# Kernel tuning notes

Hardware: AMD Instinct MI355X
Metric: run time of the kernel (lower is better)

Reference implementation:

```python
import jax, jax.numpy as jnp
import numpy as np

B, S, D, H = 2, 1024, 1024, 8
HD = D // H            # head_dim = 128
NBUCKETS = 64          # bucket_size (number of hash buckets)
NEG = -1e30


def setup_inputs() -> dict:
    key = jax.random.key(0)
    ks = jax.random.split(key, 10)
    scale = D ** -0.5
    return {
        "x": jax.random.normal(ks[0], (B, S, D), dtype=jnp.float32),
        "Wq": jax.random.normal(ks[1], (D, D), dtype=jnp.float32) * scale,
        "bq": jnp.zeros((D,), dtype=jnp.float32),
        "Wk": jax.random.normal(ks[2], (D, D), dtype=jnp.float32) * scale,
        "bk": jnp.zeros((D,), dtype=jnp.float32),
        "Wv": jax.random.normal(ks[3], (D, D), dtype=jnp.float32) * scale,
        "bv": jnp.zeros((D,), dtype=jnp.float32),
        "Wo": jax.random.normal(ks[4], (D, D), dtype=jnp.float32) * scale,
        "bo": jnp.zeros((D,), dtype=jnp.float32),
        "hash_proj": jax.random.normal(ks[5], (H, HD, NBUCKETS), dtype=jnp.float32),
    }


def reference(x, Wq, bq, Wk, bk, Wv, bv, Wo, bo, hash_proj):
    b, s, d = x.shape
    n = b * s  # buckets gather (batch, token) pairs jointly -> flatten batch into tokens

    def split_heads(y):  # [B,S,D] -> [H, B*S, HD]
        return y.reshape(b, s, H, HD).transpose(2, 0, 1, 3).reshape(H, n, HD)

    q = split_heads(x @ Wq + bq)
    k = split_heads(x @ Wk + bk)
    v = split_heads(x @ Wv + bv)

    # learned LSH routing: argmax over hash projections per head
    hash_scores = jnp.einsum('hnd,hdf->hnf', q, hash_proj)
    buckets = jnp.argmax(hash_scores, axis=-1)  # [H, N] int

    # per-bucket attention == masked dense attention with same-bucket mask
    dots = jnp.einsum('hnd,hmd->hnm', q, k) / (HD ** 0.5)  # [H,N,N]
    same = buckets[:, :, None] == buckets[:, None, :]
    attn = jax.nn.softmax(jnp.where(same, dots, NEG), axis=-1)
    o = jnp.einsum('hnm,hmd->hnd', attn, v)  # [H,N,HD]

    out = o.reshape(H, b, s, HD).transpose(1, 2, 0, 3).reshape(b, s, d)
    return out @ Wo + bo
```

## Files before the change

kernel.cpp:

```cpp
#include <hip/hip_runtime.h>
#include <stdint.h>

typedef __attribute__((ext_vector_type(8))) short short8;
typedef __attribute__((ext_vector_type(4))) short short4v;
typedef __attribute__((ext_vector_type(4))) float float4v;
typedef unsigned short u16;

#define N_TOK 2048
#define D_MODEL 1024
#define N_HEAD 8
#define HDIM 128
#define N_BUCKET 64
#define WL_CAP 2048
#define ATTN_BLOCKS 384

__device__ __forceinline__ u16 f2bf(float f) {
  uint32_t u = __float_as_uint(f);
  uint32_t r = u + 0x7fffu + ((u >> 16) & 1u);
  return (u16)(r >> 16);
}
__device__ __forceinline__ float bf2f(u16 h) {
  return __uint_as_float(((uint32_t)h) << 16);
}

__device__ __forceinline__ void async_load16(const void* g, void* l) {
  __builtin_amdgcn_global_load_lds(
      (const __attribute__((address_space(1))) void*)g,
      (__attribute__((address_space(3))) void*)l, 16, 0, 0);
}

__device__ __forceinline__ int xcd_swz(int bid, int nwg) {
  return (bid & 7) * (nwg >> 3) + (bid >> 3);
}

__global__ __launch_bounds__(256) void split_cast_kernel(
    const float* __restrict__ in, u16* __restrict__ hi, u16* __restrict__ lo,
    int n) {
  int i = blockIdx.x * 256 + threadIdx.x;
  if (i >= n) return;
  float v = in[i];
  u16 h = f2bf(v);
  hi[i] = h;
  if (lo) lo[i] = f2bf(v - bf2f(h));
}

__global__ __launch_bounds__(256) void transpose_all_kernel(
    const float* __restrict__ Wq, const float* __restrict__ Wk,
    const float* __restrict__ Wv, const float* __restrict__ Wo,
    u16* __restrict__ wqt_hi, u16* __restrict__ wqt_lo,
    u16* __restrict__ kvt, u16* __restrict__ wot) {
  __shared__ float tile[32][33];
  const int z = blockIdx.z;
  const float* in = (z == 0) ? Wq : (z == 1) ? Wk : (z == 2) ? Wv : Wo;
  u16* hi = (z == 0) ? wqt_hi
            : (z == 1) ? kvt
            : (z == 2) ? (kvt + (size_t)1024 * 1024) : wot;
  u16* lo = (z == 0) ? wqt_lo : nullptr;
  const int C = 1024, R = 1024;
  int c0 = blockIdx.x * 32, r0 = blockIdx.y * 32;
  int tx = threadIdx.x & 31, ty = threadIdx.x >> 5;
#pragma unroll
  for (int i = 0; i < 4; i++) {
    int rl = ty + i * 8;
    tile[rl][tx] = in[(size_t)(r0 + rl) * C + c0 + tx];
  }
  __syncthreads();
#pragma unroll
  for (int i = 0; i < 4; i++) {
    int cl = ty + i * 8;
    float v = tile[tx][cl];
    size_t oidx = (size_t)(c0 + cl) * R + r0 + tx;
    u16 h = f2bf(v);
    hi[oidx] = h;
    if (lo) lo[oidx] = f2bf(v - bf2f(h));
  }
}

template <int BM>
__device__ __forceinline__ void stage_tiles2(const u16* A, const u16* Bt,
                                             u16* As, u16* Bs, int bm, int bn,
                                             int K, int ko, int wave, int lane) {
  const int arow = lane >> 2;
  const int acolb = (lane & 3) * 16;
  constexpr int ACH = BM / 16;
  constexpr int PC = (ACH + 8) / 4;
#pragma unroll
  for (int cc = 0; cc < PC; cc++) {
    int idx = wave * PC + cc;
    if (idx < ACH) {
      int row = idx * 16 + arow;
      const char* g = (const char*)A + ((size_t)(bm + row) * K + ko) * 2 + acolb;
      async_load16(g, (char*)As + idx * 1024);
    } else {
      int row = (idx - ACH) * 16 + arow;
      const char* g = (const char*)Bt + ((size_t)(bn + row) * K + ko) * 2 + acolb;
      async_load16(g, (char*)Bs + (idx - ACH) * 1024);
    }
  }
}

template <int BM>
__global__ __launch_bounds__(256) void gemm_bf16_kernel(
    const u16* __restrict__ A, const u16* __restrict__ Bt,
    float* __restrict__ C, const float* __restrict__ bias,
    const float* __restrict__ bias2, u16* __restrict__ kbf,
    u16* __restrict__ vbf, int N, int K, int flags) {
  constexpr int MI = BM / 32;
  __shared__ __align__(16) u16 As[2][BM * 32];
  __shared__ __align__(16) u16 Bs[2][128 * 32];
  const int tid = threadIdx.x;
  const int wave = tid >> 6, lane = tid & 63;
  const int lhi = lane >> 4, llo = lane & 15;
  const int nbn = N >> 7;
  const int bid = xcd_swz(blockIdx.x, gridDim.x);
  const int bm = (bid / nbn) * BM;
  const int bn = (bid % nbn) << 7;
  const int wm = (BM == 128) ? (wave >> 1) * 64 : (wave & 1) * 32;
  const int wn = (BM == 128) ? (wave & 1) * 64 : (wave >> 1) * 64;

  float4v acc[MI][4];
#pragma unroll
  for (int mi = 0; mi < MI; mi++)
#pragma unroll
    for (int ni = 0; ni < 4; ni++)
#pragma unroll
      for (int r = 0; r < 4; r++) acc[mi][ni][r] = 0.f;

  stage_tiles2<BM>(A, Bt, As[0], Bs[0], bm, bn, K, 0, wave, lane);
  __syncthreads();
  const int nk = K >> 5;
  for (int t = 0; t < nk; t++) {
    const int cur = t & 1;
    if (t + 1 < nk)
      stage_tiles2<BM>(A, Bt, As[cur ^ 1], Bs[cur ^ 1], bm, bn, K,
                       (t + 1) << 5, wave, lane);
    short8 af[MI], bfr[4];
#pragma unroll
    for (int i = 0; i < MI; i++)
      af[i] = *(const short8*)&As[cur][(wm + i * 16 + llo) * 32 + lhi * 8];
#pragma unroll
    for (int i = 0; i < 4; i++)
      bfr[i] = *(const short8*)&Bs[cur][(wn + i * 16 + llo) * 32 + lhi * 8];
#pragma unroll
    for (int mi = 0; mi < MI; mi++)
#pragma unroll
      for (int ni = 0; ni < 4; ni++)
        acc[mi][ni] = __builtin_amdgcn_mfma_f32_16x16x32_bf16(af[mi], bfr[ni],
                                                              acc[mi][ni], 0, 0, 0);
    __syncthreads();
  }

#pragma unroll
  for (int mi = 0; mi < MI; mi++)
#pragma unroll
    for (int ni = 0; ni < 4; ni++) {
      int row0 = bm + wm + mi * 16 + lhi * 4;
      int col = bn + wn + ni * 16 + llo;
      if (flags & 8) {
        u16* dst = (col < 1024) ? kbf : vbf;
        int c = col & 1023;
        float bb = (col < 1024) ? bias[c] : bias2[c];
#pragma unroll
        for (int r = 0; r < 4; r++)
          dst[(size_t)(row0 + r) * 1024 + c] = f2bf(acc[mi][ni][r] + bb);
      } else {
        float bb = (flags & 2) ? bias[col] : 0.f;
        float* cp = C + (size_t)row0 * N + col;
#pragma unroll
        for (int r = 0; r < 4; r++) cp[(size_t)r * N] = acc[mi][ni][r] + bb;
      }
    }
}

__global__ __launch_bounds__(256) void gemm3_bf16_kernel(
    const u16* __restrict__ A0, const u16* __restrict__ A1,
    const u16* __restrict__ B0, const u16* __restrict__ B1,
    float* __restrict__ C, const float* __restrict__ bias,
    u16* __restrict__ bf_out, int N, int K) {
  constexpr int MI = 2;
  __shared__ __align__(16) u16 S3[2][12288];
  const int tid = threadIdx.x;
  const int wave = tid >> 6, lane = tid & 63;
  const int lhi = lane >> 4, llo = lane & 15;
  const int nbn = N >> 7;
  const int bid = xcd_swz(blockIdx.x, gridDim.x);
  const int bm = (bid / nbn) * 64;
  const int bn = (bid % nbn) << 7;
  const int wm = (wave & 1) * 32;
  const int wn = (wave >> 1) * 64;
  const int arow = lane >> 2;
  const int acolb = (lane & 3) * 16;

  float4v acc[MI][4];
#pragma unroll
  for (int mi = 0; mi < MI; mi++)
#pragma unroll
    for (int ni = 0; ni < 4; ni++)
#pragma unroll
      for (int r = 0; r < 4; r++) acc[mi][ni][r] = 0.f;

  auto stage = [&](int b, int ko) {
    char* base = (char*)&S3[b][0];
#pragma unroll
    for (int cc = 0; cc < 6; cc++) {
      int idx = wave * 6 + cc;
      const u16* src;
      int row;
      char* dst;
      if (idx < 4) {
        src = A0; row = bm + idx * 16 + arow; dst = base + idx * 1024;
      } else if (idx < 8) {
        src = A1; row = bm + (idx - 4) * 16 + arow; dst = base + 4096 + (idx - 4) * 1024;
      } else if (idx < 16) {
        src = B0; row = bn + (idx - 8) * 16 + arow; dst = base + 8192 + (idx - 8) * 1024;
      } else {
        src = B1; row = bn + (idx - 16) * 16 + arow; dst = base + 16384 + (idx - 16) * 1024;
      }
      async_load16((const char*)src + ((size_t)row * K + ko) * 2 + acolb, dst);
    }
  };

  stage(0, 0);
  __syncthreads();
  const int nk = K >> 5;
  for (int t = 0; t < nk; t++) {
    const int cur = t & 1;
    if (t + 1 < nk) stage(cur ^ 1, (t + 1) << 5);
    const u16* Sc = &S3[cur][0];
    short8 afh[MI], afl[MI], bfh[4], bfl[4];
#pragma unroll
    for (int i = 0; i < MI; i++) {
      afh[i] = *(const short8*)&Sc[(wm + i * 16 + llo) * 32 + lhi * 8];
      afl[i] = *(const short8*)&Sc[2048 + (wm + i * 16 + llo) * 32 + lhi * 8];
    }
#pragma unroll
    for (int i = 0; i < 4; i++) {
      bfh[i] = *(const short8*)&Sc[4096 + (wn + i * 16 + llo) * 32 + lhi * 8];
      bfl[i] = *(const short8*)&Sc[8192 + (wn + i * 16 + llo) * 32 + lhi * 8];
    }
#pragma unroll
    for (int mi = 0; mi < MI; mi++)
#pragma unroll
      for (int ni = 0; ni < 4; ni++)
        acc[mi][ni] = __builtin_amdgcn_mfma_f32_16x16x32_bf16(afh[mi], bfh[ni],
                                                              acc[mi][ni], 0, 0, 0);
#pragma unroll
    for (int mi = 0; mi < MI; mi++)
#pragma unroll
      for (int ni = 0; ni < 4; ni++)
        acc[mi][ni] = __builtin_amdgcn_mfma_f32_16x16x32_bf16(afh[mi], bfl[ni],
                                                              acc[mi][ni], 0, 0, 0);
#pragma unroll
    for (int mi = 0; mi < MI; mi++)
#pragma unroll
      for (int ni = 0; ni < 4; ni++)
        acc[mi][ni] = __builtin_amdgcn_mfma_f32_16x16x32_bf16(afl[mi], bfh[ni],
                                                              acc[mi][ni], 0, 0, 0);
    __syncthreads();
  }

#pragma unroll
  for (int mi = 0; mi < MI; mi++)
#pragma unroll
    for (int ni = 0; ni < 4; ni++) {
      int row0 = bm + wm + mi * 16 + lhi * 4;
      int col = bn + wn + ni * 16 + llo;
      float bb = bias[col];
#pragma unroll
      for (int r = 0; r < 4; r++) {
        float v = acc[mi][ni][r] + bb;
        C[(size_t)(row0 + r) * N + col] = v;
        bf_out[(size_t)(row0 + r) * N + col] = f2bf(v);
      }
    }
}

__global__ __launch_bounds__(256) void hash_argmax_kernel(
    const float* __restrict__ Qf, const float* __restrict__ proj,
    int* __restrict__ bucket) {
  __shared__ float sQ[64 * 128];
  __shared__ float sP[128 * 64];
  const int tid = threadIdx.x;
  const int h = blockIdx.y;
  const int n0 = blockIdx.x * 64;
#pragma unroll
  for (int p = 0; p < 8; p++) {
    int e = p * 1024 + tid * 4;
    int tok = e >> 7, d0 = e & 127;
    float4v v = *(const float4v*)&Qf[(size_t)(n0 + tok) * D_MODEL + h * HDIM + d0];
    int blk = (d0 >> 2) ^ ((tok >> 2) & 7);
    *(float4v*)&sQ[tok * 128 + blk * 4] = v;
  }
#pragma unroll
  for (int p = 0; p < 8; p++) {
    int e = p * 1024 + tid * 4;
    float4v v = *(const float4v*)&proj[(size_t)h * (HDIM * N_BUCKET) + e];
    *(float4v*)&sP[e] = v;
  }
  __syncthreads();

  const int tgrp = tid & 15, fgrp = tid >> 4;
  const int t0 = tgrp * 4, f0 = fgrp * 4;
  float accs[4][4];
#pragma unroll
  for (int i = 0; i < 4; i++)
#pragma unroll
    for (int f = 0; f < 4; f++) accs[i][f] = 0.f;

  for (int d0 = 0; d0 < 128; d0 += 4) {
    int blk = (d0 >> 2) ^ (tgrp & 7);
    float4v qv[4], pv[4];
#pragma unroll
    for (int i = 0; i < 4; i++)
      qv[i] = *(const float4v*)&sQ[(t0 + i) * 128 + blk * 4];
#pragma unroll
    for (int j = 0; j < 4; j++)
      pv[j] = *(const float4v*)&sP[(d0 + j) * 64 + f0];
#pragma unroll
    for (int i = 0; i < 4; i++)
#pragma unroll
      for (int f = 0; f < 4; f++)
        accs[i][f] += qv[i][0] * pv[0][f] + qv[i][1] * pv[1][f] +
                      qv[i][2] * pv[2][f] + qv[i][3] * pv[3][f];
  }

  __syncthreads();
  float* vals = sQ;
  int* idxs = (int*)(sQ + 64 * 17);
#pragma unroll
  for (int i = 0; i < 4; i++) {
    float bv = accs[i][0];
    int bi = f0;
#pragma unroll
    for (int f = 1; f < 4; f++)
      if (accs[i][f] > bv) { bv = accs[i][f]; bi = f0 + f; }
    vals[(t0 + i) * 17 + fgrp] = bv;
    idxs[(t0 + i) * 17 + fgrp] = bi;
  }
  __syncthreads();
  if (tid < 64) {
    float bv = vals[tid * 17];
    int bi = idxs[tid * 17];
#pragma unroll
    for (int g = 1; g < 16; g++) {
      float v = vals[tid * 17 + g];
      int id = idxs[tid * 17 + g];
      if (v > bv || (v == bv && id < bi)) { bv = v; bi = id; }
    }
    bucket[h * N_TOK + n0 + tid] = bi;
  }
}

__global__ __launch_bounds__(64) void bucket_count_kernel(
    const int* __restrict__ bucket, int* __restrict__ counts) {
  int hb = blockIdx.x;
  int h = hb >> 6, b = hb & 63;
  int lane = threadIdx.x;
  int cnt = 0;
  for (int t = 0; t < N_TOK; t += 64) {
    bool match = bucket[h * N_TOK + t + lane] == b;
    unsigned long long mask = __ballot(match);
    cnt += __popcll(mask);
  }
  if (lane == 0) counts[hb] = cnt;
}

__global__ __launch_bounds__(512) void build_wl_kernel(
    const int* __restrict__ counts, int* __restrict__ offsets,
    int* __restrict__ wl, int* __restrict__ wl_count) {
  __shared__ int sc[512];
  int tid = threadIdx.x;
  int cnt = counts[tid];
  sc[tid] = cnt;
  __syncthreads();
  for (int o = 1; o < 512; o <<= 1) {
    int v = (tid >= o) ? sc[tid - o] : 0;
    __syncthreads();
    sc[tid] += v;
    __syncthreads();
  }
  offsets[tid] = sc[tid] - cnt;
  __syncthreads();
  int nq = (cnt + 15) >> 4;
  sc[tid] = nq;
  __syncthreads();
  for (int o = 1; o < 512; o <<= 1) {
    int v = (tid >= o) ? sc[tid - o] : 0;
    __syncthreads();
    sc[tid] += v;
    __syncthreads();
  }
  int base = sc[tid] - nq;
  int h = tid >> 6, b = tid & 63;
  for (int i = 0; i < nq; i++) wl[base + i] = (h << 13) | (b << 7) | i;
  if (tid == 511) wl_count[0] = sc[511];
}

__global__ __launch_bounds__(64) void bucket_fill_kernel(
    const int* __restrict__ bucket, const int* __restrict__ offsets,
    int* __restrict__ perm) {
  int hb = blockIdx.x;
  int h = hb >> 6, b = hb & 63;
  int lane = threadIdx.x;
  int base = offsets[hb];
  for (int t = 0; t < N_TOK; t += 64) {
    int tok = t + lane;
    bool match = bucket[h * N_TOK + tok] == b;
    unsigned long long mask = __ballot(match);
    if (match) {
      int pos = base + __popcll(mask & ((1ull << lane) - 1ull));
      perm[pos] = tok;
    }
    base += __popcll(mask);
  }
}

__global__ __launch_bounds__(256) void gather_vt_kernel(
    const u16* __restrict__ vbb, const int* __restrict__ perm,
    u16* __restrict__ Vts) {
  __shared__ u16 lds[64][72];
  int bid = blockIdx.x;
  int h = bid >> 6;
  int ptile = (bid & 63) >> 1;
  int d0 = (bid & 1) * 64;
  int pos0 = ptile * 64;
  int t = threadIdx.x;
#pragma unroll
  for (int i = 0; i < 2; i++) {
    int unit = t + 256 * i;
    int p = unit >> 3, seg = unit & 7;
    int tok = perm[h * N_TOK + pos0 + p];
    short8 v = *(const short8*)&vbb[(size_t)tok * D_MODEL + h * HDIM + d0 + seg * 8];
    *(short8*)&lds[p][seg * 8] = v;
  }
  __syncthreads();
#pragma unroll
  for (int i = 0; i < 8; i++) {
    int unit = t + 256 * i;
    int drow = unit >> 5, pp = unit & 31;
    uint32_t val = (uint32_t)lds[2 * pp][drow] |
                   ((uint32_t)lds[2 * pp + 1][drow] << 16);
    uint32_t* dst = (uint32_t*)&Vts[(size_t)(h * HDIM + d0 + drow) * N_TOK + pos0];
    dst[pp] = val;
  }
}

__global__ __launch_bounds__(256) void attn_bucket_kernel(
    const u16* __restrict__ qbb, const u16* __restrict__ kbb,
    const u16* __restrict__ Vts, const int* __restrict__ perm,
    const int* __restrict__ offsets, const int* __restrict__ counts,
    const int* __restrict__ wl, const int* __restrict__ wl_count,
    u16* __restrict__ ob) {
  const int wave = threadIdx.x >> 6, lane = threadIdx.x & 63;
  const int lhi = lane >> 4, llo = lane & 15;
  const int wslot = blockIdx.x * 4 + wave;
  const int NW = ATTN_BLOCKS * 4;
  const int cnt = wl_count[0];
  __shared__ __align__(16) u16 P_lds[4][16][64];
  const float scale = 0.08838834764831845f;

  for (int e = wslot; e < cnt; e += NW) {
    int ent = wl[e];
    int h = ent >> 13, qt = ent & 127;
    int hb = (h << 6) | ((ent >> 7) & 63);
    int off = offsets[hb];
    int bs = counts[hb];
    int offh = off - h * N_TOK;
    int qbase = qt * 16;

    int qr = qbase + llo;
    int tokq = perm[off + min(qr, bs - 1)];
    const u16* qrow = &qbb[(size_t)tokq * D_MODEL + h * HDIM];
    short8 qf[4];
#pragma unroll
    for (int kf = 0; kf < 4; kf++)
      qf[kf] = *(const short8*)&qrow[kf * 32 + lhi * 8];

    float m[4], l[4];
#pragma unroll
    for (int r = 0; r < 4; r++) { m[r] = -INFINITY; l[r] = 0.f; }
    float4v accO[8];
#pragma unroll
    for (int d = 0; d < 8; d++)
#pragma unroll
      for (int r = 0; r < 4; r++) accO[d][r] = 0.f;

    for (int c0 = 0; c0 < bs; c0 += 64) {
      float4v sc[4];
#pragma unroll
      for (int nf = 0; nf < 4; nf++)
#pragma unroll
        for (int r = 0; r < 4; r++) sc[nf][r] = 0.f;
#pragma unroll
      for (int nf = 0; nf < 4; nf++) {
        int kcol = c0 + nf * 16 + llo;
        int tokk = perm[off + min(kcol, bs - 1)];
        const u16* krow = &kbb[(size_t)tokk * D_MODEL + h * HDIM];
#pragma unroll
        for (int kf = 0; kf < 4; kf++) {
          short8 kfr = *(const short8*)&krow[kf * 32 + lhi * 8];
          sc[nf] = __builtin_amdgcn_mfma_f32_16x16x32_bf16(qf[kf], kfr, sc[nf], 0, 0, 0);
        }
      }

      float tmax[4];
#pragma unroll
      for (int r = 0; r < 4; r++) tmax[r] = -INFINITY;
#pragma unroll
      for (int nf = 0; nf < 4; nf++) {
        bool valid = (c0 + nf * 16 + llo) < bs;
#pragma unroll
        for (int r = 0; r < 4; r++) {
          float v = valid ? sc[nf][r] * scale : -1e30f;
          sc[nf][r] = v;
          tmax[r] = fmaxf(tmax[r], v);
        }
      }
#pragma unroll
      for (int r = 0; r < 4; r++)
#pragma unroll
        for (int o = 1; o < 16; o <<= 1)
          tmax[r] = fmaxf(tmax[r], __shfl_xor(tmax[r], o));

      float resc[4], psum[4];
#pragma unroll
      for (int r = 0; r < 4; r++) {
        float mn = fmaxf(m[r], tmax[r]);
        resc[r] = __expf(m[r] - mn);
        m[r] = mn;
        psum[r] = 0.f;
      }
#pragma unroll
      for (int nf = 0; nf < 4; nf++)
#pragma unroll
        for (int r = 0; r < 4; r++) {
          float p = __expf(sc[nf][r] - m[r]);
          psum[r] += p;
          P_lds[wave][lhi * 4 + r][nf * 16 + llo] = f2bf(p);
        }
#pragma unroll
      for (int r = 0; r < 4; r++) {
#pragma unroll
        for (int o = 1; o < 16; o <<= 1) psum[r] += __shfl_xor(psum[r], o);
        l[r] = l[r] * resc[r] + psum[r];
      }
#pragma unroll
      for (int d = 0; d < 8; d++)
#pragma unroll
        for (int r = 0; r < 4; r++) accO[d][r] *= resc[r];

      asm volatile("s_waitcnt lgkmcnt(0)" ::: "memory");
      short8 pf[2];
#pragma unroll
      for (int k2 = 0; k2 < 2; k2++)
        pf[k2] = *(const short8*)&P_lds[wave][llo][k2 * 32 + lhi * 8];
#pragma unroll
      for (int d = 0; d < 8; d++)
#pragma unroll
        for (int k2 = 0; k2 < 2; k2++) {
          short8 vfr = *(const short8*)&Vts[(size_t)(h * HDIM + d * 16 + llo) * N_TOK +
                                            offh + c0 + k2 * 32 + lhi * 8];
          accO[d] = __builtin_amdgcn_mfma_f32_16x16x32_bf16(pf[k2], vfr, accO[d], 0, 0, 0);
        }
      asm volatile("" ::: "memory");
    }

#pragma unroll
    for (int r = 0; r < 4; r++) {
      int rl = qbase + lhi * 4 + r;
      if (rl < bs) {
        int tok = perm[off + rl];
        float inv = 1.f / l[r];
#pragma unroll
        for (int d = 0; d < 8; d++)
          ob[(size_t)tok * D_MODEL + h * HDIM + d * 16 + llo] = f2bf(accO[d][r] * inv);
      }
    }
  }
}

extern "C" void kernel_launch(void* const* d_in, const int* in_sizes, int n_in,
                              void* d_out, int out_size, void* d_ws, size_t ws_size,
                              hipStream_t stream) {
  const float* x  = (const float*)d_in[0];
  const float* Wq = (const float*)d_in[1];
  const float* bq = (const float*)d_in[2];
  const float* Wk = (const float*)d_in[3];
  const float* bk = (const float*)d_in[4];
  const float* Wv = (const float*)d_in[5];
  const float* bv = (const float*)d_in[6];
  const float* Wo = (const float*)d_in[7];
  const float* bo = (const float*)d_in[8];
  const float* hp = (const float*)d_in[9];
  float* out = (float*)d_out;

  char* ws = (char*)d_ws;
  size_t off = 0;
  auto alloc = [&](size_t b) {
    char* p = ws + off;
    off += (b + 255) & ~(size_t)255;
    return p;
  };

  const int N = N_TOK, D = D_MODEL;
  u16* xhi    = (u16*)alloc((size_t)N * D * 2);
  u16* xlo    = (u16*)alloc((size_t)N * D * 2);
  u16* wqt_hi = (u16*)alloc((size_t)D * D * 2);
  u16* wqt_lo = (u16*)alloc((size_t)D * D * 2);
  u16* kvt    = (u16*)alloc((size_t)2 * D * D * 2);
  u16* wot    = (u16*)alloc((size_t)D * D * 2);
  float* Qf   = (float*)alloc((size_t)N * D * 4);
  u16* qbb    = (u16*)alloc((size_t)N * D * 2);
  u16* kbb    = (u16*)alloc((size_t)N * D * 2);
  u16* vbb    = (u16*)alloc((size_t)N * D * 2);
  u16* Vts    = (u16*)alloc((size_t)N_HEAD * HDIM * N * 2 + 256);
  int* bucket = (int*)alloc((size_t)N_HEAD * N * 4);
  int* counts = (int*)alloc(512 * 4);
  int* offs   = (int*)alloc(512 * 4);
  int* perm   = (int*)alloc((size_t)N_HEAD * N * 4);
  int* wl     = (int*)alloc(WL_CAP * 4);
  int* wlcnt  = (int*)alloc(256);
  u16* ob     = (u16*)alloc((size_t)N * D * 2);

  const int nelem = N * D;

  split_cast_kernel<<<(nelem + 255) / 256, 256, 0, stream>>>(x, xhi, xlo, nelem);
  transpose_all_kernel<<<dim3(32, 32, 4), 256, 0, stream>>>(
      Wq, Wk, Wv, Wo, wqt_hi, wqt_lo, kvt, wot);

  gemm3_bf16_kernel<<<(N / 64) * (D / 128), 256, 0, stream>>>(
      xhi, xlo, wqt_hi, wqt_lo, Qf, bq, qbb, D, D);
  gemm_bf16_kernel<64><<<(N / 64) * (2 * D / 128), 256, 0, stream>>>(
      xhi, kvt, nullptr, bk, bv, kbb, vbb, 2 * D, D, 2 | 8);

  hash_argmax_kernel<<<dim3(N / 64, N_HEAD), 256, 0, stream>>>(Qf, hp, bucket);
  bucket_count_kernel<<<512, 64, 0, stream>>>(bucket, counts);
  build_wl_kernel<<<1, 512, 0, stream>>>(counts, offs, wl, wlcnt);
  bucket_fill_kernel<<<512, 64, 0, stream>>>(bucket, offs, perm);
  gather_vt_kernel<<<512, 256, 0, stream>>>(vbb, perm, Vts);

  attn_bucket_kernel<<<ATTN_BLOCKS, 256, 0, stream>>>(
      qbb, kbb, Vts, perm, offs, counts, wl, wlcnt, ob);

  gemm_bf16_kernel<64><<<(N / 64) * (D / 128), 256, 0, stream>>>(
      ob, wot, out, bo, nullptr, nullptr, nullptr, D, D, 2);

  (void)in_sizes; (void)n_in; (void)out_size; (void)ws_size;
}
```

Measured before the change: 131.7 us.

## Fold hash projection into Wq and merge QKV GEMM and bucket sort kernels

New measurement: 161.4 us. 1.23x slower.

```diff
diff --git a/kernel.cpp b/kernel.cpp
--- a/kernel.cpp
+++ b/kernel.cpp
@@ -47,15 +47,11 @@
 __global__ __launch_bounds__(256) void transpose_all_kernel(
     const float* __restrict__ Wq, const float* __restrict__ Wk,
     const float* __restrict__ Wv, const float* __restrict__ Wo,
-    u16* __restrict__ wqt_hi, u16* __restrict__ wqt_lo,
-    u16* __restrict__ kvt, u16* __restrict__ wot) {
+    u16* __restrict__ qkvt, u16* __restrict__ wot) {
   __shared__ float tile[32][33];
   const int z = blockIdx.z;
   const float* in = (z == 0) ? Wq : (z == 1) ? Wk : (z == 2) ? Wv : Wo;
-  u16* hi = (z == 0) ? wqt_hi
-            : (z == 1) ? kvt
-            : (z == 2) ? (kvt + (size_t)1024 * 1024) : wot;
-  u16* lo = (z == 0) ? wqt_lo : nullptr;
+  u16* hi = (z == 3) ? wot : qkvt + (size_t)z * 1024 * 1024;
   const int C = 1024, R = 1024;
   int c0 = blockIdx.x * 32, r0 = blockIdx.y * 32;
   int tx = threadIdx.x & 31, ty = threadIdx.x >> 5;
@@ -68,81 +64,120 @@
 #pragma unroll
   for (int i = 0; i < 4; i++) {
     int cl = ty + i * 8;
-    float v = tile[tx][cl];
-    size_t oidx = (size_t)(c0 + cl) * R + r0 + tx;
-    u16 h = f2bf(v);
-    hi[oidx] = h;
-    if (lo) lo[oidx] = f2bf(v - bf2f(h));
-  }
-}
-
-template <int BM>
-__device__ __forceinline__ void stage_tiles2(const u16* A, const u16* Bt,
-                                             u16* As, u16* Bs, int bm, int bn,
-                                             int K, int ko, int wave, int lane) {
-  const int arow = lane >> 2;
-  const int acolb = (lane & 3) * 16;
-  constexpr int ACH = BM / 16;
-  constexpr int PC = (ACH + 8) / 4;
-#pragma unroll
-  for (int cc = 0; cc < PC; cc++) {
-    int idx = wave * PC + cc;
-    if (idx < ACH) {
-      int row = idx * 16 + arow;
-      const char* g = (const char*)A + ((size_t)(bm + row) * K + ko) * 2 + acolb;
-      async_load16(g, (char*)As + idx * 1024);
-    } else {
-      int row = (idx - ACH) * 16 + arow;
-      const char* g = (const char*)Bt + ((size_t)(bn + row) * K + ko) * 2 + acolb;
-      async_load16(g, (char*)Bs + (idx - ACH) * 1024);
-    }
-  }
-}
-
-template <int BM>
-__global__ __launch_bounds__(256) void gemm_bf16_kernel(
+    hi[(size_t)(c0 + cl) * R + r0 + tx] = f2bf(tile[tx][cl]);
+  }
+}
+
+__global__ __launch_bounds__(256) void wqp_build_kernel(
+    const float* __restrict__ Wq, const float* __restrict__ proj,
+    const float* __restrict__ bq, u16* __restrict__ Wqpt_hi,
+    u16* __restrict__ Wqpt_lo, float* __restrict__ bias_sc) {
+  __shared__ float sW[64][128];
+  __shared__ float sPj[128][64];
+  const int tid = threadIdx.x;
+  const int rt = blockIdx.x, h = blockIdx.y;
+  const int dd0 = rt * 64;
+#pragma unroll
+  for (int p = 0; p < 8; p++) {
+    int e = p * 1024 + tid * 4;
+    int row = e >> 7, col = e & 127;
+    *(float4v*)&sW[row][col] =
+        *(const float4v*)&Wq[(size_t)(dd0 + row) * 1024 + h * HDIM + col];
+    *(float4v*)&sPj[0][0 + e] = *(const float4v*)&proj[(size_t)h * (HDIM * N_BUCKET) + e];
+  }
+  __syncthreads();
+  const int tr0 = (tid & 15) * 4, tc0 = (tid >> 4) * 4;
+  float acc[4][4];
+#pragma unroll
+  for (int i = 0; i < 4; i++)
+#pragma unroll
+    for (int j = 0; j < 4; j++) acc[i][j] = 0.f;
+  for (int dl = 0; dl < 128; dl++) {
+    float4v pv = *(const float4v*)&sPj[dl][tc0];
+#pragma unroll
+    for (int i = 0; i < 4; i++) {
+      float w = sW[tr0 + i][dl];
+#pragma unroll
+      for (int j = 0; j < 4; j++) acc[i][j] += w * pv[j];
+    }
+  }
+#pragma unroll
+  for (int j = 0; j < 4; j++) {
+    short4v ph, pl;
+#pragma unroll
+    for (int i = 0; i < 4; i++) {
+      float v = acc[i][j];
+      u16 hh = f2bf(v);
+      ph[i] = (short)hh;
+      pl[i] = (short)f2bf(v - bf2f(hh));
+    }
+    size_t ofs = (size_t)(h * 64 + tc0 + j) * 1024 + dd0 + tr0;
+    *(short4v*)&Wqpt_hi[ofs] = ph;
+    *(short4v*)&Wqpt_lo[ofs] = pl;
+  }
+  if (rt == 0 && tid < 64) {
+    float s = 0.f;
+    for (int dl = 0; dl < 128; dl++) s += bq[h * HDIM + dl] * sPj[dl][tid];
+    bias_sc[h * 64 + tid] = s;
+  }
+}
+
+__global__ __launch_bounds__(256) void qkv_gemm_kernel(
     const u16* __restrict__ A, const u16* __restrict__ Bt,
-    float* __restrict__ C, const float* __restrict__ bias,
-    const float* __restrict__ bias2, u16* __restrict__ kbf,
-    u16* __restrict__ vbf, int N, int K, int flags) {
-  constexpr int MI = BM / 32;
-  __shared__ __align__(16) u16 As[2][BM * 32];
+    const float* __restrict__ bq, const float* __restrict__ bk,
+    const float* __restrict__ bv, u16* __restrict__ qbb,
+    u16* __restrict__ kbb, u16* __restrict__ vbb) {
+  const int K = 1024;
+  __shared__ __align__(16) u16 As[2][128 * 32];
   __shared__ __align__(16) u16 Bs[2][128 * 32];
   const int tid = threadIdx.x;
   const int wave = tid >> 6, lane = tid & 63;
   const int lhi = lane >> 4, llo = lane & 15;
-  const int nbn = N >> 7;
   const int bid = xcd_swz(blockIdx.x, gridDim.x);
-  const int bm = (bid / nbn) * BM;
-  const int bn = (bid % nbn) << 7;
-  const int wm = (BM == 128) ? (wave >> 1) * 64 : (wave & 1) * 32;
-  const int wn = (BM == 128) ? (wave & 1) * 64 : (wave >> 1) * 64;
-
-  float4v acc[MI][4];
-#pragma unroll
-  for (int mi = 0; mi < MI; mi++)
+  const int bm = (bid / 24) << 7;
+  const int bn = (bid % 24) << 7;
+  const int wm = (wave >> 1) * 64;
+  const int wn = (wave & 1) * 64;
+  const int arow = lane >> 2;
+  const int acolb = (lane & 3) * 16;
+
+  float4v acc[4][4];
+#pragma unroll
+  for (int mi = 0; mi < 4; mi++)
 #pragma unroll
     for (int ni = 0; ni < 4; ni++)
 #pragma unroll
       for (int r = 0; r < 4; r++) acc[mi][ni][r] = 0.f;
 
-  stage_tiles2<BM>(A, Bt, As[0], Bs[0], bm, bn, K, 0, wave, lane);
-  __syncthreads();
-  const int nk = K >> 5;
-  for (int t = 0; t < nk; t++) {
+  auto stage = [&](int b, int ko) {
+#pragma unroll
+    for (int cc = 0; cc < 4; cc++) {
+      int idx = wave * 4 + cc;
+      if (idx < 8) {
+        int row = bm + idx * 16 + arow;
+        async_load16((const char*)A + ((size_t)row * K + ko) * 2 + acolb,
+                     (char*)&As[b][0] + idx * 1024);
+      } else {
+        int row = bn + (idx - 8) * 16 + arow;
+        async_load16((const char*)Bt + ((size_t)row * K + ko) * 2 + acolb,
+                     (char*)&Bs[b][0] + (idx - 8) * 1024);
+      }
+    }
+  };
+
+  stage(0, 0);
+  __syncthreads();
+  for (int t = 0; t < 32; t++) {
     const int cur = t & 1;
-    if (t + 1 < nk)
-      stage_tiles2<BM>(A, Bt, As[cur ^ 1], Bs[cur ^ 1], bm, bn, K,
-                       (t + 1) << 5, wave, lane);
-    short8 af[MI], bfr[4];
-#pragma unroll
-    for (int i = 0; i < MI; i++)
+    if (t + 1 < 32) stage(cur ^ 1, (t + 1) << 5);
+    short8 af[4], bfr[4];
+#pragma unroll
+    for (int i = 0; i < 4; i++) {
       af[i] = *(const short8*)&As[cur][(wm + i * 16 + llo) * 32 + lhi * 8];
-#pragma unroll
-    for (int i = 0; i < 4; i++)
       bfr[i] = *(const short8*)&Bs[cur][(wn + i * 16 + llo) * 32 + lhi * 8];
-#pragma unroll
-    for (int mi = 0; mi < MI; mi++)
+    }
+#pragma unroll
+    for (int mi = 0; mi < 4; mi++)
 #pragma unroll
       for (int ni = 0; ni < 4; ni++)
         acc[mi][ni] = __builtin_amdgcn_mfma_f32_16x16x32_bf16(af[mi], bfr[ni],
@@ -151,70 +186,59 @@
   }
 
 #pragma unroll
-  for (int mi = 0; mi < MI; mi++)
+  for (int mi = 0; mi < 4; mi++)
 #pragma unroll
     for (int ni = 0; ni < 4; ni++) {
       int row0 = bm + wm + mi * 16 + lhi * 4;
       int col = bn + wn + ni * 16 + llo;
-      if (flags & 8) {
-        u16* dst = (col < 1024) ? kbf : vbf;
-        int c = col & 1023;
-        float bb = (col < 1024) ? bias[c] : bias2[c];
-#pragma unroll
-        for (int r = 0; r < 4; r++)
-          dst[(size_t)(row0 + r) * 1024 + c] = f2bf(acc[mi][ni][r] + bb);
-      } else {
-        float bb = (flags & 2) ? bias[col] : 0.f;
-        float* cp = C + (size_t)row0 * N + col;
-#pragma unroll
-        for (int r = 0; r < 4; r++) cp[(size_t)r * N] = acc[mi][ni][r] + bb;
-      }
-    }
-}
-
-__global__ __launch_bounds__(256) void gemm3_bf16_kernel(
+      int seg = col >> 10, c = col & 1023;
+      u16* dst = (seg == 0) ? qbb : (seg == 1) ? kbb : vbb;
+      float bb = (seg == 0) ? bq[c] : (seg == 1) ? bk[c] : bv[c];
+#pragma unroll
+      for (int r = 0; r < 4; r++)
+        dst[(size_t)(row0 + r) * 1024 + c] = f2bf(acc[mi][ni][r] + bb);
+    }
+}
+
+__global__ __launch_bounds__(256) void score_argmax_kernel(
     const u16* __restrict__ A0, const u16* __restrict__ A1,
     const u16* __restrict__ B0, const u16* __restrict__ B1,
-    float* __restrict__ C, const float* __restrict__ bias,
-    u16* __restrict__ bf_out, int N, int K) {
-  constexpr int MI = 2;
-  __shared__ __align__(16) u16 S3[2][12288];
+    const float* __restrict__ bias_sc, int* __restrict__ bucket) {
+  const int K = 1024;
+  __shared__ __align__(16) u16 S[2][10240];
   const int tid = threadIdx.x;
   const int wave = tid >> 6, lane = tid & 63;
   const int lhi = lane >> 4, llo = lane & 15;
-  const int nbn = N >> 7;
   const int bid = xcd_swz(blockIdx.x, gridDim.x);
-  const int bm = (bid / nbn) * 64;
-  const int bn = (bid % nbn) << 7;
-  const int wm = (wave & 1) * 32;
+  const int bm = (bid >> 2) << 5;
+  const int bn = (bid & 3) << 7;
+  const int wm = (wave & 1) * 16;
   const int wn = (wave >> 1) * 64;
   const int arow = lane >> 2;
   const int acolb = (lane & 3) * 16;
 
-  float4v acc[MI][4];
-#pragma unroll
-  for (int mi = 0; mi < MI; mi++)
-#pragma unroll
-    for (int ni = 0; ni < 4; ni++)
-#pragma unroll
-      for (int r = 0; r < 4; r++) acc[mi][ni][r] = 0.f;
+  float4v acc[4];
+#pragma unroll
+  for (int ni = 0; ni < 4; ni++)
+#pragma unroll
+    for (int r = 0; r < 4; r++) acc[ni][r] = 0.f;
 
   auto stage = [&](int b, int ko) {
-    char* base = (char*)&S3[b][0];
-#pragma unroll
-    for (int cc = 0; cc < 6; cc++) {
-      int idx = wave * 6 + cc;
+    char* base = (char*)&S[b][0];
+#pragma unroll
+    for (int cc = 0; cc < 5; cc++) {
+      int idx = wave * 5 + cc;
       const u16* src;
       int row;
       char* dst;
-      if (idx < 4) {
+      if (idx < 2) {
         src = A0; row = bm + idx * 16 + arow; dst = base + idx * 1024;
-      } else if (idx < 8) {
-        src = A1; row = bm + (idx - 4) * 16 + arow; dst = base + 4096 + (idx - 4) * 1024;
-      } else if (idx < 16) {
-        src = B0; row = bn + (idx - 8) * 16 + arow; dst = base + 8192 + (idx - 8) * 1024;
+      } else if (idx < 4) {
+        src = A1; row = bm + (idx - 2) * 16 + arow; dst = base + 2048 + (idx - 2) * 1024;
+      } else if (idx < 12) {
+        src = B0; row = bn + (idx - 4) * 16 + arow; dst = base + 4096 + (idx - 4) * 1024;
       } else {
-        src = B1; row = bn + (idx - 16) * 16 + arow; dst = base + 16384 + (idx - 16) * 1024;
+        src = B1; row = bn + (idx - 12) * 16 + arow; dst = base + 12288 + (idx - 12) * 1024;
       }
       async_load16((const char*)src + ((size_t)row * K + ko) * 2 + acolb, dst);
     }
@@ -222,156 +246,82 @@
 
   stage(0, 0);
   __syncthreads();
-  const int nk = K >> 5;
-  for (int t = 0; t < nk; t++) {
+  for (int t = 0; t < 32; t++) {
     const int cur = t & 1;
-    if (t + 1 < nk) stage(cur ^ 1, (t + 1) << 5);
-    const u16* Sc = &S3[cur][0];
-    short8 afh[MI], afl[MI], bfh[4], bfl[4];
-#pragma unroll
-    for (int i = 0; i < MI; i++) {
-      afh[i] = *(const short8*)&Sc[(wm + i * 16 + llo) * 32 + lhi * 8];
-      afl[i] = *(const short8*)&Sc[2048 + (wm + i * 16 + llo) * 32 + lhi * 8];
-    }
+    if (t + 1 < 32) stage(cur ^ 1, (t + 1) << 5);
+    const u16* Sc = &S[cur][0];
+    short8 afh, afl, bfh[4], bfl[4];
+    afh = *(const short8*)&Sc[(wm + llo) * 32 + lhi * 8];
+    afl = *(const short8*)&Sc[1024 + (wm + llo) * 32 + lhi * 8];
 #pragma unroll
     for (int i = 0; i < 4; i++) {
-      bfh[i] = *(const short8*)&Sc[4096 + (wn + i * 16 + llo) * 32 + lhi * 8];
-      bfl[i] = *(const short8*)&Sc[8192 + (wn + i * 16 + llo) * 32 + lhi * 8];
-    }
-#pragma unroll
-    for (int mi = 0; mi < MI; mi++)
-#pragma unroll
-      for (int ni = 0; ni < 4; ni++)
-        acc[mi][ni] = __builtin_amdgcn_mfma_f32_16x16x32_bf16(afh[mi], bfh[ni],
-                                                              acc[mi][ni], 0, 0, 0);
-#pragma unroll
-    for (int mi = 0; mi < MI; mi++)
-#pragma unroll
-      for (int ni = 0; ni < 4; ni++)
-        acc[mi][ni] = __builtin_amdgcn_mfma_f32_16x16x32_bf16(afh[mi], bfl[ni],
-                                                              acc[mi][ni], 0, 0, 0);
-#pragma unroll
-    for (int mi = 0; mi < MI; mi++)
-#pragma unroll
-      for (int ni = 0; ni < 4; ni++)
-        acc[mi][ni] = __builtin_amdgcn_mfma_f32_16x16x32_bf16(afl[mi], bfh[ni],
-                                                              acc[mi][ni], 0, 0, 0);
+      bfh[i] = *(const short8*)&Sc[2048 + (wn + i * 16 + llo) * 32 + lhi * 8];
+      bfl[i] = *(const short8*)&Sc[6144 + (wn + i * 16 + llo) * 32 + lhi * 8];
+    }
+#pragma unroll
+    for (int ni = 0; ni < 4; ni++)
+      acc[ni] = __builtin_amdgcn_mfma_f32_16x16x32_bf16(afh, bfh[ni], acc[ni], 0, 0, 0);
+#pragma unroll
+    for (int ni = 0; ni < 4; ni++)
+      acc[ni] = __builtin_amdgcn_mfma_f32_16x16x32_bf16(afh, bfl[ni], acc[ni], 0, 0, 0);
+#pragma unroll
+    for (int ni = 0; ni < 4; ni++)
+      acc[ni] = __builtin_amdgcn_mfma_f32_16x16x32_bf16(afl, bfh[ni], acc[ni], 0, 0, 0);
     __syncthreads();
   }
 
-#pragma unroll
-  for (int mi = 0; mi < MI; mi++)
-#pragma unroll
-    for (int ni = 0; ni < 4; ni++) {
-      int row0 = bm + wm + mi * 16 + lhi * 4;
-      int col = bn + wn + ni * 16 + llo;
-      float bb = bias[col];
-#pragma unroll
-      for (int r = 0; r < 4; r++) {
-        float v = acc[mi][ni][r] + bb;
-        C[(size_t)(row0 + r) * N + col] = v;
-        bf_out[(size_t)(row0 + r) * N + col] = f2bf(v);
-      }
-    }
-}
-
-__global__ __launch_bounds__(256) void hash_argmax_kernel(
-    const float* __restrict__ Qf, const float* __restrict__ proj,
-    int* __restrict__ bucket) {
-  __shared__ float sQ[64 * 128];
-  __shared__ float sP[128 * 64];
+  const int head = (bn + wn) >> 6;
+  float bsc[4];
+#pragma unroll
+  for (int ni = 0; ni < 4; ni++) bsc[ni] = bias_sc[head * 64 + ni * 16 + llo];
+#pragma unroll
+  for (int r = 0; r < 4; r++) {
+    float bv = acc[0][r] + bsc[0];
+    int bi = llo;
+#pragma unroll
+    for (int ni = 1; ni < 4; ni++) {
+      float v = acc[ni][r] + bsc[ni];
+      if (v > bv) { bv = v; bi = ni * 16 + llo; }
+    }
+#pragma unroll
+    for (int o = 1; o < 16; o <<= 1) {
+      float ov = __shfl_xor(bv, o);
+      int oi = __shfl_xor(bi, o);
+      if (ov > bv || (ov == bv && oi < bi)) { bv = ov; bi = oi; }
+    }
+    if (llo == 0) bucket[head * N_TOK + bm + wm + lhi * 4 + r] = bi;
+  }
+}
+
+__device__ __forceinline__ unsigned long long match_mask(int b) {
+  unsigned long long mask = ~0ull;
+#pragma unroll
+  for (int bit = 0; bit < 6; bit++) {
+    unsigned long long vt = __ballot((b >> bit) & 1);
+    mask &= ((b >> bit) & 1) ? vt : ~vt;
+  }
+  return mask;
+}
+
+__global__ __launch_bounds__(512) void sort_kernel(
+    const int* __restrict__ bucket, int* __restrict__ counts_g,
+    int* __restrict__ offsets_g, int* __restrict__ perm,
+    int* __restrict__ wl, int* __restrict__ wl_count) {
+  __shared__ int cnt[512];
+  __shared__ int sc[512];
+  __shared__ int run[512];
   const int tid = threadIdx.x;
-  const int h = blockIdx.y;
-  const int n0 = blockIdx.x * 64;
-#pragma unroll
-  for (int p = 0; p < 8; p++) {
-    int e = p * 1024 + tid * 4;
-    int tok = e >> 7, d0 = e & 127;
-    float4v v = *(const float4v*)&Qf[(size_t)(n0 + tok) * D_MODEL + h * HDIM + d0];
-    int blk = (d0 >> 2) ^ ((tok >> 2) & 7);
-    *(float4v*)&sQ[tok * 128 + blk * 4] = v;
-  }
-#pragma unroll
-  for (int p = 0; p < 8; p++) {
-    int e = p * 1024 + tid * 4;
-    float4v v = *(const float4v*)&proj[(size_t)h * (HDIM * N_BUCKET) + e];
-    *(float4v*)&sP[e] = v;
-  }
-  __syncthreads();
-
-  const int tgrp = tid & 15, fgrp = tid >> 4;
-  const int t0 = tgrp * 4, f0 = fgrp * 4;
-  float accs[4][4];
-#pragma unroll
-  for (int i = 0; i < 4; i++)
-#pragma unroll
-    for (int f = 0; f < 4; f++) accs[i][f] = 0.f;
-
-  for (int d0 = 0; d0 < 128; d0 += 4) {
-    int blk = (d0 >> 2) ^ (tgrp & 7);
-    float4v qv[4], pv[4];
-#pragma unroll
-    for (int i = 0; i < 4; i++)
-      qv[i] = *(const float4v*)&sQ[(t0 + i) * 128 + blk * 4];
-#pragma unroll
-    for (int j = 0; j < 4; j++)
-      pv[j] = *(const float4v*)&sP[(d0 + j) * 64 + f0];
-#pragma unroll
-    for (int i = 0; i < 4; i++)
-#pragma unroll
-      for (int f = 0; f < 4; f++)
-        accs[i][f] += qv[i][0] * pv[0][f] + qv[i][1] * pv[1][f] +
-                      qv[i][2] * pv[2][f] + qv[i][3] * pv[3][f];
-  }
-
-  __syncthreads();
-  float* vals = sQ;
-  int* idxs = (int*)(sQ + 64 * 17);
-#pragma unroll
-  for (int i = 0; i < 4; i++) {
-    float bv = accs[i][0];
-    int bi = f0;
-#pragma unroll
-    for (int f = 1; f < 4; f++)
-      if (accs[i][f] > bv) { bv = accs[i][f]; bi = f0 + f; }
-    vals[(t0 + i) * 17 + fgrp] = bv;
-    idxs[(t0 + i) * 17 + fgrp] = bi;
-  }
-  __syncthreads();
-  if (tid < 64) {
-    float bv = vals[tid * 17];
-    int bi = idxs[tid * 17];
-#pragma unroll
-    for (int g = 1; g < 16; g++) {
-      float v = vals[tid * 17 + g];
-      int id = idxs[tid * 17 + g];
-      if (v > bv || (v == bv && id < bi)) { bv = v; bi = id; }
-    }
-    bucket[h * N_TOK + n0 + tid] = bi;
-  }
-}
-
-__global__ __launch_bounds__(64) void bucket_count_kernel(
-    const int* __restrict__ bucket, int* __restrict__ counts) {
-  int hb = blockIdx.x;
-  int h = hb >> 6, b = hb & 63;
-  int lane = threadIdx.x;
-  int cnt = 0;
+  const int w = tid >> 6, lane = tid & 63;
+  cnt[tid] = 0;
+  __syncthreads();
   for (int t = 0; t < N_TOK; t += 64) {
-    bool match = bucket[h * N_TOK + t + lane] == b;
-    unsigned long long mask = __ballot(match);
-    cnt += __popcll(mask);
-  }
-  if (lane == 0) counts[hb] = cnt;
-}
-
-__global__ __launch_bounds__(512) void build_wl_kernel(
-    const int* __restrict__ counts, int* __restrict__ offsets,
-    int* __restrict__ wl, int* __restrict__ wl_count) {
-  __shared__ int sc[512];
-  int tid = threadIdx.x;
-  int cnt = counts[tid];
-  sc[tid] = cnt;
+    int b = bucket[w * N_TOK + t + lane];
+    unsigned long long mask = match_mask(b);
+    if (lane == __ffsll(mask) - 1) cnt[w * 64 + b] += __popcll(mask);
+  }
+  __syncthreads();
+  int c = cnt[tid];
+  sc[tid] = c;
   __syncthreads();
   for (int o = 1; o < 512; o <<= 1) {
     int v = (tid >= o) ? sc[tid - o] : 0;
@@ -379,9 +329,12 @@
     sc[tid] += v;
     __syncthreads();
   }
-  offsets[tid] = sc[tid] - cnt;
-  __syncthreads();
-  int nq = (cnt + 15) >> 4;
+  int off0 = sc[tid] - c;
+  offsets_g[tid] = off0;
+  counts_g[tid] = c;
+  run[tid] = off0;
+  __syncthreads();
+  int nq = (c + 15) >> 4;
   sc[tid] = nq;
   __syncthreads();
   for (int o = 1; o < 512; o <<= 1) {
@@ -391,27 +344,18 @@
     __syncthreads();
   }
   int base = sc[tid] - nq;
-  int h = tid >> 6, b = tid & 63;
-  for (int i = 0; i < nq; i++) wl[base + i] = (h << 13) | (b << 7) | i;
+  int hh = tid >> 6, bb = tid & 63;
+  for (int i = 0; i < nq; i++) wl[base + i] = (hh << 13) | (bb << 7) | i;
   if (tid == 511) wl_count[0] = sc[511];
-}
-
-__global__ __launch_bounds__(64) void bucket_fill_kernel(
-    const int* __restrict__ bucket, const int* __restrict__ offsets,
-    int* __restrict__ perm) {
-  int hb = blockIdx.x;
-  int h = hb >> 6, b = hb & 63;
-  int lane = threadIdx.x;
-  int base = offsets[hb];
+  __syncthreads();
   for (int t = 0; t < N_TOK; t += 64) {
     int tok = t + lane;
-    bool match = bucket[h * N_TOK + tok] == b;
-    unsigned long long mask = __ballot(match);
-    if (match) {
-      int pos = base + __popcll(mask & ((1ull << lane) - 1ull));
-      perm[pos] = tok;
-    }
-    base += __popcll(mask);
+    int b = bucket[w * N_TOK + tok];
+    unsigned long long mask = match_mask(b);
+    int lower = __popcll(mask & ((1ull << lane) - 1ull));
+    int pos = run[w * 64 + b] + lower;
+    perm[pos] = tok;
+    if (lane == __ffsll(mask) - 1) run[w * 64 + b] += __popcll(mask);
   }
 }
 
@@ -486,11 +430,11 @@
       for (int r = 0; r < 4; r++) accO[d][r] = 0.f;
 
     for (int c0 = 0; c0 < bs; c0 += 64) {
-      float4v sc[4];
+      float4v scv[4];
 #pragma unroll
       for (int nf = 0; nf < 4; nf++)
 #pragma unroll
-        for (int r = 0; r < 4; r++) sc[nf][r] = 0.f;
+        for (int r = 0; r < 4; r++) scv[nf][r] = 0.f;
 #pragma unroll
       for (int nf = 0; nf < 4; nf++) {
         int kcol = c0 + nf * 16 + llo;
@@ -499,7 +443,7 @@
 #pragma unroll
         for (int kf = 0; kf < 4; kf++) {
           short8 kfr = *(const short8*)&krow[kf * 32 + lhi * 8];
-          sc[nf] = __builtin_amdgcn_mfma_f32_16x16x32_bf16(qf[kf], kfr, sc[nf], 0, 0, 0);
+          scv[nf] = __builtin_amdgcn_mfma_f32_16x16x32_bf16(qf[kf], kfr, scv[nf], 0, 0, 0);
         }
       }
 
@@ -511,8 +455,8 @@
         bool valid = (c0 + nf * 16 + llo) < bs;
 #pragma unroll
         for (int r = 0; r < 4; r++) {
-          float v = valid ? sc[nf][r] * scale : -1e30f;
-          sc[nf][r] = v;
+          float v = valid ? scv[nf][r] * scale : -1e30f;
+          scv[nf][r] = v;
           tmax[r] = fmaxf(tmax[r], v);
         }
       }
@@ -534,7 +478,7 @@
       for (int nf = 0; nf < 4; nf++)
 #pragma unroll
         for (int r = 0; r < 4; r++) {
-          float p = __expf(sc[nf][r] - m[r]);
+          float p = __expf(scv[nf][r] - m[r]);
           psum[r] += p;
           P_lds[wave][lhi * 4 + r][nf * 16 + llo] = f2bf(p);
         }
@@ -577,6 +521,81 @@
       }
     }
   }
+}
+
+__global__ __launch_bounds__(256) void gemm_out_kernel(
+    const u16* __restrict__ A, const u16* __restrict__ Bt,
+    float* __restrict__ C, const float* __restrict__ bias) {
+  const int K = 1024, N = 1024;
+  __shared__ __align__(16) u16 As[2][64 * 32];
+  __shared__ __align__(16) u16 Bs[2][128 * 32];
+  const int tid = threadIdx.x;
+  const int wave = tid >> 6, lane = tid & 63;
+  const int lhi = lane >> 4, llo = lane & 15;
+  const int bid = xcd_swz(blockIdx.x, gridDim.x);
+  const int bm = (bid >> 3) * 64;
+  const int bn = (bid & 7) << 7;
+  const int wm = (wave & 1) * 32;
+  const int wn = (wave >> 1) * 64;
+  const int arow = lane >> 2;
+  const int acolb = (lane & 3) * 16;
+
+  float4v acc[2][4];
+#pragma unroll
+  for (int mi = 0; mi < 2; mi++)
+#pragma unroll
+    for (int ni = 0; ni < 4; ni++)
+#pragma unroll
+      for (int r = 0; r < 4; r++) acc[mi][ni][r] = 0.f;
+
+  auto stage = [&](int b, int ko) {
+#pragma unroll
+    for (int cc = 0; cc < 3; cc++) {
+      int idx = wave * 3 + cc;
+      if (idx < 4) {
+        int row = bm + idx * 16 + arow;
+        async_load16((const char*)A + ((size_t)row * K + ko) * 2 + acolb,
+                     (char*)&As[b][0] + idx * 1024);
+      } else {
+        int row = bn + (idx - 4) * 16 + arow;
+        async_load16((const char*)Bt + ((size_t)row * K + ko) * 2 + acolb,
+                     (char*)&Bs[b][0] + (idx - 4) * 1024);
+      }
+    }
+  };
+
+  stage(0, 0);
+  __syncthreads();
+  for (int t = 0; t < 32; t++) {
+    const int cur = t & 1;
+    if (t + 1 < 32) stage(cur ^ 1, (t + 1) << 5);
+    short8 af[2], bfr[4];
+#pragma unroll
+    for (int i = 0; i < 2; i++)
+      af[i] = *(const short8*)&As[cur][(wm + i * 16 + llo) * 32 + lhi * 8];
+#pragma unroll
+    for (int i = 0; i < 4; i++)
+      bfr[i] = *(const short8*)&Bs[cur][(wn + i * 16 + llo) * 32 + lhi * 8];
+#pragma unroll
+    for (int mi = 0; mi < 2; mi++)
+#pragma unroll
+      for (int ni = 0; ni < 4; ni++)
+        acc[mi][ni] = __builtin_amdgcn_mfma_f32_16x16x32_bf16(af[mi], bfr[ni],
+                                                              acc[mi][ni], 0, 0, 0);
+    __syncthreads();
+  }
+
+#pragma unroll
+  for (int mi = 0; mi < 2; mi++)
+#pragma unroll
+    for (int ni = 0; ni < 4; ni++) {
+      int row0 = bm + wm + mi * 16 + lhi * 4;
+      int col = bn + wn + ni * 16 + llo;
+      float bb = bias[col];
+#pragma unroll
+      for (int r = 0; r < 4; r++)
+        C[(size_t)(row0 + r) * N + col] = acc[mi][ni][r] + bb;
+    }
 }
 
 extern "C" void kernel_launch(void* const* d_in, const int* in_sizes, int n_in,
@@ -603,47 +622,41 @@
   };
 
   const int N = N_TOK, D = D_MODEL;
-  u16* xhi    = (u16*)alloc((size_t)N * D * 2);
-  u16* xlo    = (u16*)alloc((size_t)N * D * 2);
-  u16* wqt_hi = (u16*)alloc((size_t)D * D * 2);
-  u16* wqt_lo = (u16*)alloc((size_t)D * D * 2);
-  u16* kvt    = (u16*)alloc((size_t)2 * D * D * 2);
-  u16* wot    = (u16*)alloc((size_t)D * D * 2);
-  float* Qf   = (float*)alloc((size_t)N * D * 4);
-  u16* qbb    = (u16*)alloc((size_t)N * D * 2);
-  u16* kbb    = (u16*)alloc((size_t)N * D * 2);
-  u16* vbb    = (u16*)alloc((size_t)N * D * 2);
-  u16* Vts    = (u16*)alloc((size_t)N_HEAD * HDIM * N * 2 + 256);
-  int* bucket = (int*)alloc((size_t)N_HEAD * N * 4);
-  int* counts = (int*)alloc(512 * 4);
-  int* offs   = (int*)alloc(512 * 4);
-  int* perm   = (int*)alloc((size_t)N_HEAD * N * 4);
-  int* wl     = (int*)alloc(WL_CAP * 4);
-  int* wlcnt  = (int*)alloc(256);
-  u16* ob     = (u16*)alloc((size_t)N * D * 2);
+  u16* xhi     = (u16*)alloc((size_t)N * D * 2);
+  u16* xlo     = (u16*)alloc((size_t)N * D * 2);
+  u16* qkvt    = (u16*)alloc((size_t)3 * D * D * 2);
+  u16* wot     = (u16*)alloc((size_t)D * D * 2);
+  u16* Wqpt_hi = (u16*)alloc((size_t)512 * D * 2);
+  u16* Wqpt_lo = (u16*)alloc((size_t)512 * D * 2);
+  float* biasc = (float*)alloc(512 * 4);
+  u16* qbb     = (u16*)alloc((size_t)N * D * 2);
+  u16* kbb     = (u16*)alloc((size_t)N * D * 2);
+  u16* vbb     = (u16*)alloc((size_t)N * D * 2);
+  u16* Vts     = (u16*)alloc((size_t)N_HEAD * HDIM * N * 2 + 256);
+  int* bucket  = (int*)alloc((size_t)N_HEAD * N * 4);
+  int* counts  = (int*)alloc(512 * 4);
+  int* offs    = (int*)alloc(512 * 4);
+  int* perm    = (int*)alloc((size_t)N_HEAD * N * 4);
+  int* wl      = (int*)alloc(WL_CAP * 4);
+  int* wlcnt   = (int*)alloc(256);
+  u16* ob      = (u16*)alloc((size_t)N * D * 2);
 
   const int nelem = N * D;
 
   split_cast_kernel<<<(nelem + 255) / 256, 256, 0, stream>>>(x, xhi, xlo, nelem);
-  transpose_all_kernel<<<dim3(32, 32, 4), 256, 0, stream>>>(
-      Wq, Wk, Wv, Wo, wqt_hi, wqt_lo, kvt, wot);
-
-  gemm3_bf16_kernel<<<(N / 64) * (D / 128), 256, 0, stream>>>(
-      xhi, xlo, wqt_hi, wqt_lo, Qf, bq, qbb, D, D);
-  gemm_bf16_kernel<64><<<(N / 64) * (2 * D / 128), 256, 0, stream>>>(
-      xhi, kvt, nullptr, bk, bv, kbb, vbb, 2 * D, D, 2 | 8);
-
-  hash_argmax_kernel<<<dim3(N / 64, N_HEAD), 256, 0, stream>>>(Qf, hp, bucket);
-  bucket_count_kernel<<<512, 64, 0, stream>>>(bucket, counts);
-  build_wl_kernel<<<1, 512, 0, stream>>>(counts, offs, wl, wlcnt);
-  bucket_fill_kernel<<<512, 64, 0, stream>>>(bucket, offs, perm);
+  transpose_all_kernel<<<dim3(32, 32, 4), 256, 0, stream>>>(Wq, Wk, Wv, Wo, qkvt, wot);
+  wqp_build_kernel<<<dim3(16, 8), 256, 0, stream>>>(Wq, hp, bq, Wqpt_hi, Wqpt_lo, biasc);
+
+  qkv_gemm_kernel<<<384, 256, 0, stream>>>(xhi, qkvt, bq, bk, bv, qbb, kbb, vbb);
+  score_argmax_kernel<<<256, 256, 0, stream>>>(xhi, xlo, Wqpt_hi, Wqpt_lo, biasc, bucket);
+
+  sort_kernel<<<1, 512, 0, stream>>>(bucket, counts, offs, perm, wl, wlcnt);
   gather_vt_kernel<<<512, 256, 0, stream>>>(vbb, perm, Vts);
 
   attn_bucket_kernel<<<ATTN_BLOCKS, 256, 0, stream>>>(
       qbb, kbb, Vts, perm, offs, counts, wl, wlcnt, ob);
 
-  gemm_bf16_kernel<64><<<(N / 64) * (D / 128), 256, 0, stream>>>(
-      ob, wot, out, bo, nullptr, nullptr, nullptr, D, D, 2);
+  gemm_out_kernel<<<256, 256, 0, stream>>>(ob, wot, out, bo);
 
   (void)in_sizes; (void)n_in; (void)out_size; (void)ws_size;
 }
```
